# Kernel optimization log

Hardware: AMD Instinct MI355X
Metric: run time of the kernel (lower is better)

## Reference

```python
import jax, jax.numpy as jnp
import numpy as np

BN_EPS = 1e-5
NUM_HEADS = 8


def _bn(x, g, b, m, v):
    # eval-mode BatchNorm2d on NCHW
    inv = g / jnp.sqrt(v + BN_EPS)
    return x * inv[None, :, None, None] + (b - m * inv)[None, :, None, None]


def _l2norm_complex(t):
    # torch F.normalize(dim=-1) on complex: divide by L2 norm of magnitudes
    nrm = jnp.sqrt(jnp.sum(jnp.abs(t) ** 2, axis=-1, keepdims=True))
    return t / jnp.maximum(nrm, 1e-12)


def setup_inputs() -> dict:
    key = jax.random.key(0)
    ks = jax.random.split(key, 16)
    b, n, c = 8, 4096, 512
    dd = c // 2  # 256
    inp = {}
    inp['x'] = jax.random.normal(ks[0], (b, n, c), dtype=jnp.float32)
    inp['conv2_w'] = jax.random.normal(ks[1], (dd, c, 3, 3), dtype=jnp.float32) * 0.02
    inp['conv2_b'] = jax.random.normal(ks[2], (dd,), dtype=jnp.float32) * 0.02
    inp['bn2_g'] = jnp.ones((dd,), jnp.float32)
    inp['bn2_b'] = jnp.zeros((dd,), jnp.float32)
    inp['bn2_m'] = jax.random.normal(ks[3], (dd,), dtype=jnp.float32) * 0.1
    inp['bn2_v'] = jax.random.uniform(ks[4], (dd,), jnp.float32, 0.5, 1.5)
    inp['temperature'] = jnp.ones((NUM_HEADS, 1, 1), jnp.float32)
    hid = dd // 16  # 16
    inp['w1_w'] = jax.random.normal(ks[5], (hid, dd), dtype=jnp.float32) * 0.05
    inp['w1_b'] = jax.random.normal(ks[6], (hid,), dtype=jnp.float32) * 0.02
    inp['bnw_g'] = jnp.ones((hid,), jnp.float32)
    inp['bnw_b'] = jnp.zeros((hid,), jnp.float32)
    inp['bnw_m'] = jax.random.normal(ks[7], (hid,), dtype=jnp.float32) * 0.1
    inp['bnw_v'] = jax.random.uniform(ks[8], (hid,), jnp.float32, 0.5, 1.5)
    inp['w2_w'] = jax.random.normal(ks[9], (dd, hid), dtype=jnp.float32) * 0.05
    inp['w2_b'] = jax.random.normal(ks[10], (dd,), dtype=jnp.float32) * 0.02
    inp['proj_w'] = jax.random.normal(ks[11], (c, c), dtype=jnp.float32) * 0.02
    inp['proj_b'] = jax.random.normal(ks[12], (c,), dtype=jnp.float32) * 0.02
    return inp


def reference(x, conv2_w, conv2_b, bn2_g, bn2_b, bn2_m, bn2_v, temperature,
              w1_w, w1_b, bnw_g, bnw_b, bnw_m, bnw_v, w2_w, w2_b,
              proj_w, proj_b):
    b, n, c = x.shape
    h = w = int(round(n ** 0.5))
    x2d = x.reshape(b, h, w, c).transpose(0, 3, 1, 2)  # NCHW

    # conv2: 3x3 dilated (dilation=3, padding=3) -> BN -> ReLU
    conv2 = jax.lax.conv_general_dilated(
        x2d, conv2_w, window_strides=(1, 1), padding=((3, 3), (3, 3)),
        rhs_dilation=(3, 3), dimension_numbers=('NCHW', 'OIHW', 'NCHW'))
    conv2 = jax.nn.relu(_bn(conv2 + conv2_b[None, :, None, None], bn2_g, bn2_b, bn2_m, bn2_v))

    dd = conv2.shape[1]
    f = jnp.fft.fft2(conv2)  # q_f_2 = k_f_2 = v_f_2 = tepqkv (all identical)

    cph = dd // NUM_HEADS
    qkv = f.reshape(b, NUM_HEADS, cph, h * w)  # b head c (h w)
    qn = _l2norm_complex(qkv)  # q and k are identical after normalization

    # complex attention: (b,head,c,c)
    attn = jnp.einsum('bhcn,bhdn->bhcd', qn, qn) * temperature[None]
    attn = jax.lax.complex(jax.nn.softmax(attn.real, axis=-1),
                           jax.nn.softmax(attn.imag, axis=-1))
    out = jnp.einsum('bhcd,bhdn->bhcn', attn, qkv)
    # ifft2 over last two dims (c, h*w) as in the original code
    out_f2 = jnp.abs(jnp.fft.ifft2(out)).reshape(b, dd, h, w)

    # conv gating branch on real part of fft
    r = f.real
    g1 = jax.nn.relu(_bn(jnp.einsum('bchw,oc->bohw', r, w1_w) + w1_b[None, :, None, None],
                         bnw_g, bnw_b, bnw_m, bnw_v))
    gate = jax.nn.sigmoid(jnp.einsum('bchw,oc->bohw', g1, w2_w) + w2_b[None, :, None, None])
    out_l2 = jnp.abs(jnp.fft.ifft2(gate * f))

    out2 = jnp.concatenate([out_f2, out_l2], axis=1) + x2d
    F2 = jnp.einsum('bchw,oc->bohw', out2, proj_w) + proj_b[None, :, None, None]
    return F2.transpose(0, 2, 3, 1).reshape(b, n, c)
```

## Files before the change

### kernel.cpp

```cpp
#include <hip/hip_runtime.h>

#define NB 8
#define NC 512
#define ND 256
#define NP 4096
#define NHD 8
#define TWO_PI 6.2831853071795864f
#define FPITCH 65
#define HPAD 70
#define NSPL 16

typedef short bf16x8 __attribute__((ext_vector_type(8)));
typedef float f32x4 __attribute__((ext_vector_type(4)));

__device__ __forceinline__ unsigned short f2bf(float f) {
    unsigned u = __float_as_uint(f);
    u += 0x7FFFu + ((u >> 16) & 1u);
    return (unsigned short)(u >> 16);
}
__device__ __forceinline__ float bf2f(unsigned short u) {
    return __uint_as_float((unsigned)u << 16);
}

__device__ __forceinline__ void load_lds16(const void* g, void* l) {
// ... 64 lines not shown
    if (MODE == 0) {
        __syncthreads();
        #pragma unroll
        for (int k2 = 0; k2 < 8; ++k2) {
            int idx = r*FPITCH + t8 + 8*k2;
            Re[idx] = a[k2].x; Im[idx] = a[k2].y;
        }
    } else {
        #pragma unroll
        for (int k2 = 0; k2 < 8; ++k2) {
            int kq = t8 + 8*k2;
            gout[r + 64*kq] = make_float2(a[k2].x*scale, a[k2].y*scale);
        }
    }
    __syncthreads();
}

template<int S, int MODE>
__device__ void fft64_cols(float* Re, float* Im, const float* twc, const float* tws,
                           int tid, float* gre, float* gim, unsigned short* goutr,
                           float scale, float* ss)
{
    int col = tid & 63;
    int t8  = tid >> 6;
    float2 v[8];
    __syncthreads();
    #pragma unroll
    for (int m = 0; m < 8; ++m) {
        int idx = (8*m + t8)*FPITCH + col;
        v[m] = make_float2(Re[idx], Im[idx]);
    }
    dft8<S>(v);
    #pragma unroll
    for (int k1 = 1; k1 < 8; ++k1) {
        int mm = (t8*k1) & 63;
        v[k1] = cmulf(v[k1], make_float2(twc[mm], (float)S*tws[mm]));
    }
    __syncthreads();
    #pragma unroll
    for (int k1 = 0; k1 < 8; ++k1) {
        int idx = (k1*8 + t8)*FPITCH + col;
        Re[idx] = v[k1].x; Im[idx] = v[k1].y;
    }
    __syncthreads();
    float2 a[8];
    #pragma unroll
    for (int m = 0; m < 8; ++m) {
        int idx = (t8*8 + m)*FPITCH + col;
        a[m] = make_float2(Re[idx], Im[idx]);
    }
    dft8<S>(a);
    if (MODE <= 1) {
        __syncthreads();
        #pragma unroll
        for (int k2 = 0; k2 < 8; ++k2) {
            int row = t8 + 8*k2;
            float2 rv = a[k2];
            if (MODE == 1) {
                float sv, cv;
                __sincosf((TWO_PI/4096.f) * (float)(row*col), &sv, &cv);
                rv = cmulf(rv, make_float2(cv, (float)S*sv));
            }
            int idx = row*FPITCH + col;
            Re[idx] = rv.x; Im[idx] = rv.y;
        }
    } else if (MODE == 2) {
        #pragma unroll
        for (int k2 = 0; k2 < 8; ++k2) {
            int row = t8 + 8*k2;
            *ss += a[k2].x*a[k2].x + a[k2].y*a[k2].y;
            gre[row*64 + col] = a[k2].x*scale;
            gim[row*64 + col] = a[k2].y*scale;
        }
    } else {
        #pragma unroll
        for (int k2 = 0; k2 < 8; ++k2) {
            int row = t8 + 8*k2;
            goutr[row*64 + col] = f2bf(scale * sqrtf(a[k2].x*a[k2].x + a[k2].y*a[k2].y));
        }
    }
    __syncthreads();
}

__global__ __launch_bounds__(256) void k_wconv(const float* __restrict__ w, unsigned short* __restrict__ wB) {
    int idx = blockIdx.x*256 + threadIdx.x;
    if (idx >= 9*NC*ND) return;
    int i = idx & 511;
    int rest = idx >> 9;
    int o = rest & 255;
    int t = rest >> 8;
    wB[idx] = f2bf(w[(o*NC + i)*9 + t]);
}

__global__ __launch_bounds__(256) void k_wproj(const float* __restrict__ w, unsigned short* __restrict__ wb) {
    int i = blockIdx.x*256 + threadIdx.x;
    wb[i] = f2bf(w[i]);
}

__global__ __launch_bounds__(256) void k_xpad(const float* __restrict__ x, unsigned short* __restrict__ xpad) {
    int idx = blockIdx.x*256 + threadIdx.x;
    int c8 = idx & 63;
    int rest = idx >> 6;
    int wp = rest % HPAD;
    int rest2 = rest / HPAD;
    int hp = rest2 % HPAD;
    int b = rest2 / HPAD;
    int h = hp - 3, w = wp - 3;
    bf16x8 v = {0,0,0,0,0,0,0,0};
    if (((unsigned)h) < 64u && ((unsigned)w) < 64u) {
        const float* s = x + (((size_t)b*NP + h*64 + w)*NC + c8*8);
        float4 f0 = *(const float4*)(s);
        float4 f1 = *(const float4*)(s + 4);
        v[0]=(short)f2bf(f0.x); v[1]=(short)f2bf(f0.y); v[2]=(short)f2bf(f0.z); v[3]=(short)f2bf(f0.w);
        v[4]=(short)f2bf(f1.x); v[5]=(short)f2bf(f1.y); v[6]=(short)f2bf(f1.z); v[7]=(short)f2bf(f1.w);
    }
    *(bf16x8*)(xpad + ((size_t)(b*HPAD*HPAD) + hp*HPAD + wp)*NC + c8*8) = v;
}

__global__ __launch_bounds__(256, 2) void k_conv_mfma(
        const unsigned short* __restrict__ xpad, const unsigned short* __restrict__ wB,
        const float* __restrict__ cbias, const float* __restrict__ bg, const float* __restrict__ bb,
        const float* __restrict__ bm, const float* __restrict__ bv, float* __restrict__ out)
{
    __shared__ short Als[2][8192];
    __shared__ short Bls[2][8192];
    int tid = threadIdx.x;
    int p0 = blockIdx.x * 128;
    int o0 = blockIdx.y * 128;
    int b  = blockIdx.z;
    int lane = tid & 63;
    int wv = tid >> 6;
    int wr = wv >> 1, wc = wv & 1;
    int ln = lane & 15, kq = lane >> 4;
    int kqs = kq ^ ((ln >> 1) & 3);

    f32x4 acc[4][4];
    #pragma unroll
    for (int i = 0; i < 4; ++i)
        #pragma unroll
        for (int j = 0; j < 4; ++j)
            acc[i][j] = (f32x4){0.f, 0.f, 0.f, 0.f};

    int r0 = tid >> 2;
    int c16 = tid & 3;
    int c16s = c16 ^ ((r0 >> 1) & 3);
    int pA0 = p0 + r0, pA1 = p0 + 64 + r0;
    int h0 = pA0 >> 6, w0c = pA0 & 63;
    int h1 = pA1 >> 6, w1c = pA1 & 63;
    const unsigned short* xb = xpad + (size_t)b*(HPAD*HPAD)*NC;
    int oB0 = o0 + r0, oB1 = o0 + 64 + r0;
    short* AlsD0 = &Als[0][tid*8];
    short* AlsD1 = &Als[0][2048 + tid*8];
    short* BlsD0 = &Bls[0][tid*8];
    short* BlsD1 = &Bls[0][2048 + tid*8];

    auto stage = [&](int it) {
        int buf = it & 1;
        int tap = it >> 3;
        int kc  = (it & 7) << 6;
        int q   = (tap*11) >> 5;
        int dh  = q*3, dw = (tap - q*3)*3;
        const unsigned short* a0 = xb + ((size_t)((h0 + dh)*HPAD + (w0c + dw)))*NC + kc + c16s*8;
        const unsigned short* a1 = xb + ((size_t)((h1 + dh)*HPAD + (w1c + dw)))*NC + kc + c16s*8;
        const unsigned short* b0 = wB + ((size_t)(tap*ND + oB0))*NC + kc + c16s*8;
        const unsigned short* b1 = wB + ((size_t)(tap*ND + oB1))*NC + kc + c16s*8;
        int bo = buf ? 8192 : 0;
        load_lds16(a0,      AlsD0 + bo);
        load_lds16(a1,      AlsD1 + bo);
        load_lds16(a0 + 32, AlsD0 + bo + 4096);
        load_lds16(a1 + 32, AlsD1 + bo + 4096);
        load_lds16(b0,      BlsD0 + bo);
        load_lds16(b1,      BlsD1 + bo);
        load_lds16(b0 + 32, BlsD0 + bo + 4096);
        load_lds16(b1 + 32, BlsD1 + bo + 4096);
    };

    stage(0);
    #pragma unroll 2
    for (int it = 0; it < 72; ++it) {
        int buf = it & 1;
        asm volatile("s_waitcnt vmcnt(0)" ::: "memory");
        __builtin_amdgcn_s_barrier();
        __builtin_amdgcn_sched_barrier(0);
        if (it + 1 < 72) stage(it + 1);
        #pragma unroll
        for (int ks = 0; ks < 2; ++ks) {
            bf16x8 af[4], bfr[4];
            #pragma unroll
            for (int mi = 0; mi < 4; ++mi)
                af[mi] = *(const bf16x8*)&Als[buf][ks*4096 + (wr*64 + mi*16 + ln)*32 + kqs*8];
            #pragma unroll
            for (int ni = 0; ni < 4; ++ni)
                bfr[ni] = *(const bf16x8*)&Bls[buf][ks*4096 + (wc*64 + ni*16 + ln)*32 + kqs*8];
            #pragma unroll
            for (int mi = 0; mi < 4; ++mi)
                #pragma unroll
                for (int ni = 0; ni < 4; ++ni)
                    acc[mi][ni] = __builtin_amdgcn_mfma_f32_16x16x32_bf16(af[mi], bfr[ni], acc[mi][ni], 0, 0, 0);
        }
    }

    #pragma unroll
    for (int ni = 0; ni < 4; ++ni) {
        int o = o0 + wc*64 + ni*16 + ln;
        float inv = bg[o] * rsqrtf(bv[o] + 1e-5f);
        float beta = bb[o] - bm[o]*inv;
        float cbo = cbias[o];
        #pragma unroll
        for (int mi = 0; mi < 4; ++mi) {
            int p = p0 + wr*64 + mi*16 + kq*4;
            f32x4 v = acc[mi][ni];
            float4 rv;
            rv.x = fmaxf((v[0] + cbo)*inv + beta, 0.f);
            rv.y = fmaxf((v[1] + cbo)*inv + beta, 0.f);
            rv.z = fmaxf((v[2] + cbo)*inv + beta, 0.f);
            rv.w = fmaxf((v[3] + cbo)*inv + beta, 0.f);
            *(float4*)(out + ((size_t)(b*ND + o))*NP + p) = rv;
        }
    }
}

__global__ __launch_bounds__(512) void k_fft2_fwd(const float* __restrict__ src, float* __restrict__ fRe,
                                                  float* __restrict__ fIm, float* __restrict__ nrm) {
    __shared__ float Re[64*FPITCH];
    __shared__ float Im[64*FPITCH];
    __shared__ float twc[64], tws[64];
    __shared__ float part[8];
    int tid = threadIdx.x;
    size_t img = blockIdx.x;
    const float* s = src + img*4096;
    if (tid < 64) { float sv, cv; __sincosf(TWO_PI*(float)tid/64.f, &sv, &cv); twc[tid]=cv; tws[tid]=sv; }
    for (int i = tid; i < 4096; i += 512) {
        Re[(i>>6)*FPITCH + (i&63)] = s[i];
        Im[(i>>6)*FPITCH + (i&63)] = 0.f;
    }
    fft64_rows<-1,0>(Re, Im, twc, tws, tid, nullptr, 1.f);
    float ssl = 0.f;
    fft64_cols<-1,2>(Re, Im, twc, tws, tid, fRe + img*4096, fIm + img*4096, nullptr, 1.f, &ssl);
    #pragma unroll
    for (int off = 32; off > 0; off >>= 1) ssl += __shfl_down(ssl, off, 64);
    if ((tid & 63) == 0) part[tid >> 6] = ssl;
    __syncthreads();
    if (tid == 0) {
        float t = part[0]+part[1]+part[2]+part[3]+part[4]+part[5]+part[6]+part[7];
        nrm[img] = fmaxf(sqrtf(t), 1e-12f);
    }
}

__global__ __launch_bounds__(512) void k_ifft_row4096(const float* __restrict__ fRe,
        const float* __restrict__ fIm, float2* __restrict__ Z) {
    __shared__ float Re[64*FPITCH];
    __shared__ float Im[64*FPITCH];
    __shared__ float twc[64], tws[64];
    int tid = threadIdx.x;
    size_t img = blockIdx.x;
    const float* sr = fRe + img*4096;
    const float* si = fIm + img*4096;
    if (tid < 64) { float sv, cv; __sincosf(TWO_PI*(float)tid/64.f, &sv, &cv); twc[tid]=cv; tws[tid]=sv; }
    for (int i = tid; i < 4096; i += 512) {
        Re[(i>>6)*FPITCH + (i&63)] = sr[i];
        Im[(i>>6)*FPITCH + (i&63)] = si[i];
    }
    fft64_cols<1,1>(Re, Im, twc, tws, tid, nullptr, nullptr, nullptr, 1.f, nullptr);
    fft64_rows<1,1>(Re, Im, twc, tws, tid, Z + img*4096, 1.f/4096.f);
}

__global__ __launch_bounds__(512) void k_ifft2_abs_gated(const float* __restrict__ fRe,
        const float* __restrict__ fIm, const float* __restrict__ g1, const float* __restrict__ w2,
        const float* __restrict__ w2b, unsigned short* __restrict__ out) {
    __shared__ float Re[64*FPITCH];
    __shared__ float Im[64*FPITCH];
    __shared__ float twc[64], tws[64];
    int tid = threadIdx.x;
    size_t img = blockIdx.x;
    int b = (int)(img >> 8), ch = (int)(img & 255);
    const float* sr = fRe + img*4096;
    const float* si = fIm + img*4096;
    const float* g1b = g1 + (size_t)b*NP*16;
    float4 wv0 = *(const float4*)(w2 + ch*16);
    float4 wv1 = *(const float4*)(w2 + ch*16 + 4);
    float4 wv2 = *(const float4*)(w2 + ch*16 + 8);
    float4 wv3 = *(const float4*)(w2 + ch*16 + 12);
    float w2bias = w2b[ch];
    if (tid < 64) { float sv, cv; __sincosf(TWO_PI*(float)tid/64.f, &sv, &cv); twc[tid]=cv; tws[tid]=sv; }
    for (int i = tid; i < 4096; i += 512) {
        const float* gp = g1b + (size_t)i*16;
        float4 q0 = *(const float4*)(gp);
        float4 q1 = *(const float4*)(gp + 4);
        float4 q2 = *(const float4*)(gp + 8);
        float4 q3 = *(const float4*)(gp + 12);
        float acc = w2bias
            + wv0.x*q0.x + wv0.y*q0.y + wv0.z*q0.z + wv0.w*q0.w
            + wv1.x*q1.x + wv1.y*q1.y + wv1.z*q1.z + wv1.w*q1.w
            + wv2.x*q2.x + wv2.y*q2.y + wv2.z*q2.z + wv2.w*q2.w
            + wv3.x*q3.x + wv3.y*q3.y + wv3.z*q3.z + wv3.w*q3.w;
        float gate = 1.f / (1.f + __expf(-acc));
        Re[(i>>6)*FPITCH + (i&63)] = gate*sr[i];
        Im[(i>>6)*FPITCH + (i&63)] = gate*si[i];
    }
    fft64_rows<1,0>(Re, Im, twc, tws, tid, nullptr, 1.f);
    fft64_cols<1,3>(Re, Im, twc, tws, tid, nullptr, nullptr, out + img*4096, 1.f/4096.f, nullptr);
}

__global__ __launch_bounds__(256) void k_gram(const float* __restrict__ fRe, const float* __restrict__ fIm,
                                              float2* __restrict__ Gpart) {
    __shared__ short FrP[32*136];
    __shared__ short FiP[32*136];
    int split = blockIdx.x;
    int bh = blockIdx.y;
    int b = bh >> 3, h = bh & 7;
    int tid = threadIdx.x;
    int lane = tid & 63;
    int wv = tid >> 6;
    int cr = (wv >> 1) * 16, dc = (wv & 1) * 16;
    int ln = lane & 15, kq = lane >> 4;
    int r = tid >> 3;
    int g = tid & 7;
    const float* fRb = fRe + ((size_t)(b*ND + h*32) + r)*NP + split*256 + g*8;
    const float* fIb = fIm + ((size_t)(b*ND + h*32) + r)*NP + split*256 + g*8;
    short* wFr = FrP + r*136 + g*16;
    short* wFi = FiP + r*136 + g*16;

    f32x4 arr = {0.f,0.f,0.f,0.f}, aii = {0.f,0.f,0.f,0.f};
    f32x4 ari = {0.f,0.f,0.f,0.f}, air = {0.f,0.f,0.f,0.f};

    for (int chunk = 0; chunk < 4; ++chunk) {
        float4 v0 = *(const float4*)(fRb + chunk*64);
        float4 v1 = *(const float4*)(fRb + chunk*64 + 4);
        float4 w0 = *(const float4*)(fIb + chunk*64);
        float4 w1 = *(const float4*)(fIb + chunk*64 + 4);
        __syncthreads();
        float vr[8] = {v0.x,v0.y,v0.z,v0.w,v1.x,v1.y,v1.z,v1.w};
        float vi[8] = {w0.x,w0.y,w0.z,w0.w,w1.x,w1.y,w1.z,w1.w};
        bf16x8 r0v, r1v, i0v, i1v;
        #pragma unroll
        for (int j = 0; j < 4; ++j) {
            unsigned short hb;
            hb = f2bf(vr[j]);   r0v[2*j] = (short)hb; r0v[2*j+1] = (short)f2bf(vr[j]   - bf2f(hb));
            hb = f2bf(vr[4+j]); r1v[2*j] = (short)hb; r1v[2*j+1] = (short)f2bf(vr[4+j] - bf2f(hb));
            hb = f2bf(vi[j]);   i0v[2*j] = (short)hb; i0v[2*j+1] = (short)f2bf(vi[j]   - bf2f(hb));
            hb = f2bf(vi[4+j]); i1v[2*j] = (short)hb; i1v[2*j+1] = (short)f2bf(vi[4+j] - bf2f(hb));
        }
        *(bf16x8*)(wFr)     = r0v;
        *(bf16x8*)(wFr + 8) = r1v;
        *(bf16x8*)(wFi)     = i0v;
        *(bf16x8*)(wFi + 8) = i1v;
        __syncthreads();
        const short* aRp = FrP + (cr + ln)*136;
        const short* aIp = FiP + (cr + ln)*136;
        const short* bRp = FrP + (dc + ln)*136;
        const short* bIp = FiP + (dc + ln)*136;
        #pragma unroll
        for (int s = 0; s < 4; ++s) {
            int ko = s*32 + kq*8;
            bf16x8 aR = *(const bf16x8*)(aRp + ko);
            bf16x8 aI = *(const bf16x8*)(aIp + ko);
            bf16x8 bR = *(const bf16x8*)(bRp + ko);
            bf16x8 bI = *(const bf16x8*)(bIp + ko);
            arr = __builtin_amdgcn_mfma_f32_16x16x32_bf16(aR, bR, arr, 0, 0, 0);
            aii = __builtin_amdgcn_mfma_f32_16x16x32_bf16(aI, bI, aii, 0, 0, 0);
            ari = __builtin_amdgcn_mfma_f32_16x16x32_bf16(aR, bI, ari, 0, 0, 0);
            air = __builtin_amdgcn_mfma_f32_16x16x32_bf16(aI, bR, air, 0, 0, 0);
        }
    }
    float2* gout = Gpart + ((size_t)bh*NSPL + split)*1024;
    #pragma unroll
    for (int j = 0; j < 4; ++j) {
        int c = cr + kq*4 + j;
        int d = dc + ln;
        gout[c*32 + d] = make_float2(arr[j] - aii[j], ari[j] + air[j]);
    }
}

__global__ __launch_bounds__(256) void k_attn(const float2* __restrict__ Gpart, const float* __restrict__ nrm,
                                              const float* __restrict__ temp, float2* __restrict__ Ap) {
    int bh = blockIdx.x;
    int b = bh >> 3, h = bh & 7;
    int tid = threadIdx.x;
    __shared__ float2 Sm[32][33];
    __shared__ float twc[32], tws[32];
    if (tid < 32) { float sv, cv; __sincosf(TWO_PI*(float)tid/32.f, &sv, &cv); twc[tid]=cv; tws[tid]=sv; }
    const float* nb = nrm + b*ND + h*32;
    float tv = temp[h];
    const float2* gp = Gpart + (size_t)bh*NSPL*1024;
    #pragma unroll
    for (int j = 0; j < 4; ++j) {
        int e = tid*4 + j;
        int c = e >> 5, d = e & 31;
        float2 s = make_float2(0.f, 0.f);
        for (int sp = 0; sp < NSPL; ++sp) { float2 v = gp[sp*1024 + e]; s.x += v.x; s.y += v.y; }
        float sc = tv / (nb[c]*nb[d]);
        Sm[c][d] = make_float2(s.x*sc, s.y*sc);
    }
    __syncthreads();
    if (tid < 32) {
        float mr = -1e30f, mi = -1e30f;
        for (int d = 0; d < 32; ++d) { float2 v = Sm[tid][d]; mr = fmaxf(mr, v.x); mi = fmaxf(mi, v.y); }
        float sr = 0.f, si = 0.f;
        for (int d = 0; d < 32; ++d) {
            float2 v = Sm[tid][d];
            v.x = __expf(v.x - mr); v.y = __expf(v.y - mi);
            sr += v.x; si += v.y;
            Sm[tid][d] = v;
        }
        float ir = 1.f/sr, ii = 1.f/si;
        for (int d = 0; d < 32; ++d) { float2 v = Sm[tid][d]; Sm[tid][d] = make_float2(v.x*ir, v.y*ii); }
    }
    __syncthreads();
    float2* ap = Ap + (size_t)bh*1024;
    #pragma unroll
    for (int j = 0; j < 4; ++j) {
        int e = tid*4 + j;
        int k = e >> 5, d = e & 31;
        float2 acc = make_float2(0.f, 0.f);
        for (int c = 0; c < 32; ++c) {
            int m = (c*k) & 31;
            float2 w = make_float2(twc[m], tws[m]);
            float2 v = Sm[c][d];
            acc.x += w.x*v.x - w.y*v.y;
            acc.y += w.x*v.y + w.y*v.x;
        }
        ap[e] = make_float2(acc.x*(1.f/32.f), acc.y*(1.f/32.f));
    }
}

__global__ __launch_bounds__(256) void k_outf2(const float2* __restrict__ Ap, const float2* __restrict__ Z,
                                               unsigned short* __restrict__ outf2) {
    __shared__ short Are[32*136], Aim[32*136];
    __shared__ short Bre[64*136], Bim[64*136];
    int nchunk = blockIdx.x, bh = blockIdx.y;
    int b = bh >> 3, h = bh & 7;
    int n0 = nchunk * 64;
    int tid = threadIdx.x;
    int lane = tid & 63;
    int wv = tid >> 6;
    int ln = lane & 15, kq = lane >> 4;

    const float2* ap = Ap + (size_t)bh*1024;
    #pragma unroll
    for (int j = 0; j < 4; ++j) {
        int e = tid*4 + j;
        int c = e >> 5, d = e & 31;
        float2 a = ap[e];
        unsigned short rh = f2bf(a.x); unsigned short rl = f2bf(a.x - bf2f(rh));
        unsigned short ih = f2bf(a.y); unsigned short il = f2bf(a.y - bf2f(ih));
        short* pr = Are + c*136 + 4*d;
        short* pi = Aim + c*136 + 4*d;
        pr[0]=(short)rh; pr[1]=(short)rh; pr[2]=(short)rl; pr[3]=(short)rl;
        pi[0]=(short)ih; pi[1]=(short)ih; pi[2]=(short)il; pi[3]=(short)il;
    }
    const float2* zb = Z + ((size_t)(b*ND + h*32))*NP + n0;
    #pragma unroll
    for (int j = 0; j < 8; ++j) {
        int e = tid + 256*j;
        int d = e >> 6, n = e & 63;
        float2 z = zb[(size_t)d*NP + n];
        unsigned short rh = f2bf(z.x); unsigned short rl = f2bf(z.x - bf2f(rh));
        unsigned short ih = f2bf(z.y); unsigned short il = f2bf(z.y - bf2f(ih));
        short* pr = Bre + n*136 + 4*d;
        short* pi = Bim + n*136 + 4*d;
        pr[0]=(short)rh; pr[1]=(short)rl; pr[2]=(short)rh; pr[3]=(short)rl;
        pi[0]=(short)ih; pi[1]=(short)il; pi[2]=(short)ih; pi[3]=(short)il;
    }
    __syncthreads();

    f32x4 arr[2], aii[2], ari[2], air[2];
    #pragma unroll
    for (int mt = 0; mt < 2; ++mt) {
        arr[mt] = (f32x4){0.f,0.f,0.f,0.f}; aii[mt] = (f32x4){0.f,0.f,0.f,0.f};
        ari[mt] = (f32x4){0.f,0.f,0.f,0.f}; air[mt] = (f32x4){0.f,0.f,0.f,0.f};
    }
    const short* bRrow = Bre + (wv*16 + ln)*136;
    const short* bIrow = Bim + (wv*16 + ln)*136;
    #pragma unroll
    for (int s = 0; s < 4; ++s) {
        int ko = s*32 + kq*8;
        bf16x8 bR = *(const bf16x8*)(bRrow + ko);
        bf16x8 bI = *(const bf16x8*)(bIrow + ko);
        #pragma unroll
        for (int mt = 0; mt < 2; ++mt) {
            bf16x8 aR = *(const bf16x8*)(Are + (mt*16 + ln)*136 + ko);
            bf16x8 aI = *(const bf16x8*)(Aim + (mt*16 + ln)*136 + ko);
            arr[mt] = __builtin_amdgcn_mfma_f32_16x16x32_bf16(aR, bR, arr[mt], 0, 0, 0);
            aii[mt] = __builtin_amdgcn_mfma_f32_16x16x32_bf16(aI, bI, aii[mt], 0, 0, 0);
            ari[mt] = __builtin_amdgcn_mfma_f32_16x16x32_bf16(aR, bI, ari[mt], 0, 0, 0);
            air[mt] = __builtin_amdgcn_mfma_f32_16x16x32_bf16(aI, bR, air[mt], 0, 0, 0);
        }
    }
    #pragma unroll
    for (int mt = 0; mt < 2; ++mt)
        #pragma unroll
        for (int j = 0; j < 4; ++j) {
            int c = mt*16 + kq*4 + j;
            float re = arr[mt][j] - aii[mt][j];
            float im = ari[mt][j] + air[mt][j];
            outf2[((size_t)(b*ND + h*32 + c))*NP + n0 + wv*16 + ln] = f2bf(sqrtf(re*re + im*im));
        }
}

__global__ __launch_bounds__(256) void k_g1(const float* __restrict__ fRe, const float* __restrict__ w1,
        const float* __restrict__ w1b, const float* __restrict__ gg, const float* __restrict__ gb,
        const float* __restrict__ gm, const float* __restrict__ gv, float* __restrict__ g1)
{
    int pc = blockIdx.x, b = blockIdx.y;
    int tid = threadIdx.x;
    __shared__ float w1s[16*256];
    for (int i = tid; i < 4096; i += 256) w1s[i] = w1[i];
    __syncthreads();
    int p = pc*256 + tid;
    const float* fb = fRe + (size_t)b*ND*NP + p;
    float acc[16];
    #pragma unroll
    for (int j = 0; j < 16; ++j) acc[j] = 0.f;
    for (int i = 0; i < 256; ++i) {
        float v = fb[(size_t)i*NP];
        #pragma unroll
        for (int j = 0; j < 16; ++j) acc[j] += w1s[j*256 + i] * v;
    }
    float* go = g1 + ((size_t)b*NP + p)*16;
    float4 o4[4];
    #pragma unroll
    for (int j = 0; j < 16; ++j) {
        float inv = gg[j]*rsqrtf(gv[j] + 1e-5f);
        float val = (acc[j] + w1b[j])*inv + (gb[j] - gm[j]*inv);
        ((float*)o4)[j] = fmaxf(val, 0.f);
    }
    *(float4*)(go)      = o4[0];
    *(float4*)(go + 4)  = o4[1];
    *(float4*)(go + 8)  = o4[2];
    *(float4*)(go + 12) = o4[3];
}

__global__ __launch_bounds__(256) void k_prep(const unsigned short* __restrict__ outf2b,
        const unsigned short* __restrict__ outl2b, const float* __restrict__ x,
        unsigned short* __restrict__ A)
{
    int tid = threadIdx.x;
    int p = blockIdx.x*64 + (tid >> 2);
    int cs = blockIdx.y*64 + (tid & 3)*16;
    int b  = blockIdx.z;
    const unsigned short* src = (cs < ND) ? (outf2b + ((size_t)(b*ND) + cs)*NP + p)
                                          : (outl2b + ((size_t)(b*ND) + (cs - ND))*NP + p);
    float av[16];
    #pragma unroll
    for (int j = 0; j < 16; ++j) av[j] = bf2f(src[(size_t)j*NP]);
    const float* xp = x + ((size_t)(b*NP) + p)*NC + cs;
    #pragma unroll
    for (int j = 0; j < 4; ++j) {
        float4 xv = *(const float4*)(xp + j*4);
        av[j*4+0] += xv.x; av[j*4+1] += xv.y; av[j*4+2] += xv.z; av[j*4+3] += xv.w;
    }
    bf16x8 v0, v1;
    #pragma unroll
    for (int j = 0; j < 8; ++j) { v0[j] = (short)f2bf(av[j]); v1[j] = (short)f2bf(av[8+j]); }
    unsigned short* ap = A + ((size_t)(b*NP) + p)*NC + cs;
    *(bf16x8*)(ap) = v0;
    *(bf16x8*)(ap + 8) = v1;
}

__global__ __launch_bounds__(256, 2) void k_projm(
        const unsigned short* __restrict__ A, const unsigned short* __restrict__ Bw,
        const float* __restrict__ pb, float* __restrict__ out)
{
    __shared__ short Als[2][8192];
    __shared__ short Bls[2][8192];
    int tid = threadIdx.x;
    int p0 = blockIdx.x * 128;
    int o0 = blockIdx.y * 128;
    int b  = blockIdx.z;
    int lane = tid & 63;
    int wv = tid >> 6;
    int wr = wv >> 1, wc = wv & 1;
    int ln = lane & 15, kq = lane >> 4;
    int kqs = kq ^ ((ln >> 1) & 3);

    f32x4 acc[4][4];
    #pragma unroll
    for (int i = 0; i < 4; ++i)
        #pragma unroll
        for (int j = 0; j < 4; ++j)
            acc[i][j] = (f32x4){0.f, 0.f, 0.f, 0.f};

    int r0 = tid >> 2;
    int c16 = tid & 3;
    int c16s = c16 ^ ((r0 >> 1) & 3);
    const unsigned short* ga0 = A + ((size_t)(b*NP) + p0 + r0)*NC + c16s*8;
    const unsigned short* ga1 = A + ((size_t)(b*NP) + p0 + 64 + r0)*NC + c16s*8;
    const unsigned short* gb0 = Bw + (size_t)(o0 + r0)*NC + c16s*8;
    const unsigned short* gb1 = Bw + (size_t)(o0 + 64 + r0)*NC + c16s*8;
    short* AlsD0 = &Als[0][tid*8];
    short* AlsD1 = &Als[0][2048 + tid*8];
    short* BlsD0 = &Bls[0][tid*8];
    short* BlsD1 = &Bls[0][2048 + tid*8];

    auto stage = [&](int it) {
        int buf = it & 1;
        int kc = it << 6;
        int bo = buf ? 8192 : 0;
        load_lds16(ga0 + kc,      AlsD0 + bo);
        load_lds16(ga1 + kc,      AlsD1 + bo);
        load_lds16(ga0 + kc + 32, AlsD0 + bo + 4096);
        load_lds16(ga1 + kc + 32, AlsD1 + bo + 4096);
        load_lds16(gb0 + kc,      BlsD0 + bo);
        load_lds16(gb1 + kc,      BlsD1 + bo);
        load_lds16(gb0 + kc + 32, BlsD0 + bo + 4096);
        load_lds16(gb1 + kc + 32, BlsD1 + bo + 4096);
    };

    stage(0);
    #pragma unroll 2
    for (int it = 0; it < 8; ++it) {
        int buf = it & 1;
        asm volatile("s_waitcnt vmcnt(0)" ::: "memory");
        __builtin_amdgcn_s_barrier();
        __builtin_amdgcn_sched_barrier(0);
        if (it + 1 < 8) stage(it + 1);
        #pragma unroll
        for (int ks = 0; ks < 2; ++ks) {
            bf16x8 af[4], bfr[4];
            #pragma unroll
            for (int mi = 0; mi < 4; ++mi)
                af[mi] = *(const bf16x8*)&Als[buf][ks*4096 + (wr*64 + mi*16 + ln)*32 + kqs*8];
            #pragma unroll
            for (int ni = 0; ni < 4; ++ni)
                bfr[ni] = *(const bf16x8*)&Bls[buf][ks*4096 + (wc*64 + ni*16 + ln)*32 + kqs*8];
            #pragma unroll
            for (int mi = 0; mi < 4; ++mi)
                #pragma unroll
                for (int ni = 0; ni < 4; ++ni)
                    acc[mi][ni] = __builtin_amdgcn_mfma_f32_16x16x32_bf16(af[mi], bfr[ni], acc[mi][ni], 0, 0, 0);
        }
    }

    #pragma unroll
    for (int ni = 0; ni < 4; ++ni) {
        int o = o0 + wc*64 + ni*16 + ln;
        float bias = pb[o];
        #pragma unroll
        for (int mi = 0; mi < 4; ++mi) {
            int p = p0 + wr*64 + mi*16 + kq*4;
            f32x4 v = acc[mi][ni];
            float* op = out + ((size_t)(b*NP) + p)*NC + o;
            op[0]        = v[0] + bias;
            op[NC]       = v[1] + bias;
            op[2*NC]     = v[2] + bias;
            op[3*(size_t)NC] = v[3] + bias;
        }
    }
}

extern "C" void kernel_launch(void* const* d_in, const int* in_sizes, int n_in,
                              void* d_out, int out_size, void* d_ws, size_t ws_size,
                              hipStream_t stream)
{
    const float* x      = (const float*)d_in[0];
    const float* conv_w = (const float*)d_in[1];
    const float* conv_b = (const float*)d_in[2];
    const float* bn2g   = (const float*)d_in[3];
    const float* bn2b   = (const float*)d_in[4];
    const float* bn2m   = (const float*)d_in[5];
    const float* bn2v   = (const float*)d_in[6];
    const float* temp   = (const float*)d_in[7];
    const float* w1w    = (const float*)d_in[8];
    const float* w1b    = (const float*)d_in[9];
    const float* bnwg   = (const float*)d_in[10];
    const float* bnwb   = (const float*)d_in[11];
    const float* bnwm   = (const float*)d_in[12];
    const float* bnwv   = (const float*)d_in[13];
    const float* w2w    = (const float*)d_in[14];
    const float* w2b    = (const float*)d_in[15];
    const float* projw  = (const float*)d_in[16];
    const float* projb  = (const float*)d_in[17];
    float* out = (float*)d_out;

    char* ws = (char*)d_ws;
    unsigned short* wB = (unsigned short*)(ws);
    float*  nrm   = (float*)(ws);
    float2* Ap    = (float2*)(ws + 8192 + 4194304);
    float*  g1    = (float*)(ws + 8192 + 4194304 + 524288);
    char* base = ws + 6823936;
    float*  conv  = (float*)(base);
    unsigned short* outf2b = (unsigned short*)(base);
    float* fRe = (float*)(base + 33554432);
    float* fIm = (float*)(base + 33554432 + 33554432);
    unsigned short* xpad = (unsigned short*)(base + 33554432);
    char* zbase = base + 33554432 + 67108864;
    float2* Gpart = (float2*)(zbase);
    float2* Z     = (float2*)(zbase);
    unsigned short* pwb = (unsigned short*)(zbase);
    unsigned short* Abf = (unsigned short*)(zbase + 4194304);
    unsigned short* outl2b = (unsigned short*)(zbase + 37748736);

    k_wconv<<<dim3(4608), 256, 0, stream>>>(conv_w, wB);
    k_xpad<<<dim3(9800), 256, 0, stream>>>(x, xpad);
    k_conv_mfma<<<dim3(32, 2, 8), 256, 0, stream>>>(xpad, wB, conv_b, bn2g, bn2b, bn2m, bn2v, conv);
    k_fft2_fwd<<<dim3(2048), 512, 0, stream>>>(conv, fRe, fIm, nrm);
    k_gram<<<dim3(NSPL, 64), 256, 0, stream>>>(fRe, fIm, Gpart);
    k_attn<<<dim3(64), 256, 0, stream>>>(Gpart, nrm, temp, Ap);
    k_ifft_row4096<<<dim3(2048), 512, 0, stream>>>(fRe, fIm, Z);
    k_outf2<<<dim3(64, 64), 256, 0, stream>>>(Ap, Z, outf2b);
    k_g1<<<dim3(16, 8), 256, 0, stream>>>(fRe, w1w, w1b, bnwg, bnwb, bnwm, bnwv, g1);
    k_ifft2_abs_gated<<<dim3(2048), 512, 0, stream>>>(fRe, fIm, g1, w2w, w2b, outl2b);
    k_wproj<<<dim3(1024), 256, 0, stream>>>(projw, pwb);
    k_prep<<<dim3(64, 8, 8), 256, 0, stream>>>(outf2b, outl2b, x, Abf);
    k_projm<<<dim3(32, 4, 8), 256, 0, stream>>>(Abf, pwb, projb, out);
}
```

Baseline: 425.5 us.

## Merge independent small kernels into block-range dispatched launches

Result: slower. 446.9 us (+5.0%).

```diff
diff --git a/kernel.cpp b/kernel.cpp
--- a/kernel.cpp
+++ b/kernel.cpp
@@ -170,39 +170,42 @@
     __syncthreads();
 }
 
-__global__ __launch_bounds__(256) void k_wconv(const float* __restrict__ w, unsigned short* __restrict__ wB) {
-    int idx = blockIdx.x*256 + threadIdx.x;
-    if (idx >= 9*NC*ND) return;
-    int i = idx & 511;
-    int rest = idx >> 9;
-    int o = rest & 255;
-    int t = rest >> 8;
-    wB[idx] = f2bf(w[(o*NC + i)*9 + t]);
-}
-
-__global__ __launch_bounds__(256) void k_wproj(const float* __restrict__ w, unsigned short* __restrict__ wb) {
-    int i = blockIdx.x*256 + threadIdx.x;
-    wb[i] = f2bf(w[i]);
-}
-
-__global__ __launch_bounds__(256) void k_xpad(const float* __restrict__ x, unsigned short* __restrict__ xpad) {
-    int idx = blockIdx.x*256 + threadIdx.x;
-    int c8 = idx & 63;
-    int rest = idx >> 6;
-    int wp = rest % HPAD;
-    int rest2 = rest / HPAD;
-    int hp = rest2 % HPAD;
-    int b = rest2 / HPAD;
-    int h = hp - 3, w = wp - 3;
-    bf16x8 v = {0,0,0,0,0,0,0,0};
-    if (((unsigned)h) < 64u && ((unsigned)w) < 64u) {
-        const float* s = x + (((size_t)b*NP + h*64 + w)*NC + c8*8);
-        float4 f0 = *(const float4*)(s);
-        float4 f1 = *(const float4*)(s + 4);
-        v[0]=(short)f2bf(f0.x); v[1]=(short)f2bf(f0.y); v[2]=(short)f2bf(f0.z); v[3]=(short)f2bf(f0.w);
-        v[4]=(short)f2bf(f1.x); v[5]=(short)f2bf(f1.y); v[6]=(short)f2bf(f1.z); v[7]=(short)f2bf(f1.w);
-    }
-    *(bf16x8*)(xpad + ((size_t)(b*HPAD*HPAD) + hp*HPAD + wp)*NC + c8*8) = v;
+__global__ __launch_bounds__(256) void k_pre(const float* __restrict__ cw, const float* __restrict__ pw,
+        const float* __restrict__ x, unsigned short* __restrict__ wB,
+        unsigned short* __restrict__ pwb, unsigned short* __restrict__ xpad)
+{
+    int bid = blockIdx.x;
+    int tid = threadIdx.x;
+    if (bid < 4608) {
+        int idx = bid*256 + tid;
+        if (idx >= 9*NC*ND) return;
+        int i = idx & 511;
+        int rest = idx >> 9;
+        int o = rest & 255;
+        int t = rest >> 8;
+        wB[idx] = f2bf(cw[(o*NC + i)*9 + t]);
+    } else if (bid < 5632) {
+        int i = (bid - 4608)*256 + tid;
+        pwb[i] = f2bf(pw[i]);
+    } else {
+        int idx = (bid - 5632)*256 + tid;
+        int c8 = idx & 63;
+        int rest = idx >> 6;
+        int wp = rest % HPAD;
+        int rest2 = rest / HPAD;
+        int hp = rest2 % HPAD;
+        int b = rest2 / HPAD;
+        int h = hp - 3, w = wp - 3;
+        bf16x8 v = {0,0,0,0,0,0,0,0};
+        if (((unsigned)h) < 64u && ((unsigned)w) < 64u) {
+            const float* s = x + (((size_t)b*NP + h*64 + w)*NC + c8*8);
+            float4 f0 = *(const float4*)(s);
+            float4 f1 = *(const float4*)(s + 4);
+            v[0]=(short)f2bf(f0.x); v[1]=(short)f2bf(f0.y); v[2]=(short)f2bf(f0.z); v[3]=(short)f2bf(f0.w);
+            v[4]=(short)f2bf(f1.x); v[5]=(short)f2bf(f1.y); v[6]=(short)f2bf(f1.z); v[7]=(short)f2bf(f1.w);
+        }
+        *(bf16x8*)(xpad + ((size_t)(b*HPAD*HPAD) + hp*HPAD + wp)*NC + c8*8) = v;
+    }
 }
 
 __global__ __launch_bounds__(256, 2) void k_conv_mfma(
@@ -335,180 +338,211 @@
     }
 }
 
-__global__ __launch_bounds__(512) void k_ifft_row4096(const float* __restrict__ fRe,
-        const float* __restrict__ fIm, float2* __restrict__ Z) {
-    __shared__ float Re[64*FPITCH];
-    __shared__ float Im[64*FPITCH];
-    __shared__ float twc[64], tws[64];
+__global__ __launch_bounds__(256) void k_gram_g1(const float* __restrict__ fRe, const float* __restrict__ fIm,
+        float2* __restrict__ Gpart, const float* __restrict__ w1, const float* __restrict__ w1b,
+        const float* __restrict__ gg, const float* __restrict__ gb, const float* __restrict__ gm,
+        const float* __restrict__ gv, float* __restrict__ g1)
+{
+    __shared__ __align__(16) float smemF[4352];
+    int bid = blockIdx.x;
     int tid = threadIdx.x;
-    size_t img = blockIdx.x;
-    const float* sr = fRe + img*4096;
-    const float* si = fIm + img*4096;
-    if (tid < 64) { float sv, cv; __sincosf(TWO_PI*(float)tid/64.f, &sv, &cv); twc[tid]=cv; tws[tid]=sv; }
-    for (int i = tid; i < 4096; i += 512) {
-        Re[(i>>6)*FPITCH + (i&63)] = sr[i];
-        Im[(i>>6)*FPITCH + (i&63)] = si[i];
-    }
-    fft64_cols<1,1>(Re, Im, twc, tws, tid, nullptr, nullptr, nullptr, 1.f, nullptr);
-    fft64_rows<1,1>(Re, Im, twc, tws, tid, Z + img*4096, 1.f/4096.f);
-}
-
-__global__ __launch_bounds__(512) void k_ifft2_abs_gated(const float* __restrict__ fRe,
-        const float* __restrict__ fIm, const float* __restrict__ g1, const float* __restrict__ w2,
-        const float* __restrict__ w2b, unsigned short* __restrict__ out) {
-    __shared__ float Re[64*FPITCH];
-    __shared__ float Im[64*FPITCH];
-    __shared__ float twc[64], tws[64];
+    if (bid < 1024) {
+        short* FrP = (short*)smemF;
+        short* FiP = ((short*)smemF) + 32*136;
+        int split = bid & 15;
+        int bh = bid >> 4;
+        int b = bh >> 3, h = bh & 7;
+        int lane = tid & 63;
+        int wv = tid >> 6;
+        int cr = (wv >> 1) * 16, dc = (wv & 1) * 16;
+        int ln = lane & 15, kq = lane >> 4;
+        int r = tid >> 3;
+        int g = tid & 7;
+        const float* fRb = fRe + ((size_t)(b*ND + h*32) + r)*NP + split*256 + g*8;
+        const float* fIb = fIm + ((size_t)(b*ND + h*32) + r)*NP + split*256 + g*8;
+        short* wFr = FrP + r*136 + g*16;
+        short* wFi = FiP + r*136 + g*16;
+
+        f32x4 arr = {0.f,0.f,0.f,0.f}, aii = {0.f,0.f,0.f,0.f};
+        f32x4 ari = {0.f,0.f,0.f,0.f}, air = {0.f,0.f,0.f,0.f};
+
+        for (int chunk = 0; chunk < 4; ++chunk) {
+            float4 v0 = *(const float4*)(fRb + chunk*64);
+            float4 v1 = *(const float4*)(fRb + chunk*64 + 4);
+            float4 w0 = *(const float4*)(fIb + chunk*64);
+            float4 w1v = *(const float4*)(fIb + chunk*64 + 4);
+            __syncthreads();
+            float vr[8] = {v0.x,v0.y,v0.z,v0.w,v1.x,v1.y,v1.z,v1.w};
+            float vi[8] = {w0.x,w0.y,w0.z,w0.w,w1v.x,w1v.y,w1v.z,w1v.w};
+            bf16x8 r0v, r1v, i0v, i1v;
+            #pragma unroll
+            for (int j = 0; j < 4; ++j) {
+                unsigned short hb;
+                hb = f2bf(vr[j]);   r0v[2*j] = (short)hb; r0v[2*j+1] = (short)f2bf(vr[j]   - bf2f(hb));
+                hb = f2bf(vr[4+j]); r1v[2*j] = (short)hb; r1v[2*j+1] = (short)f2bf(vr[4+j] - bf2f(hb));
+                hb = f2bf(vi[j]);   i0v[2*j] = (short)hb; i0v[2*j+1] = (short)f2bf(vi[j]   - bf2f(hb));
+                hb = f2bf(vi[4+j]); i1v[2*j] = (short)hb; i1v[2*j+1] = (short)f2bf(vi[4+j] - bf2f(hb));
+            }
+            *(bf16x8*)(wFr)     = r0v;
+            *(bf16x8*)(wFr + 8) = r1v;
+            *(bf16x8*)(wFi)     = i0v;
+            *(bf16x8*)(wFi + 8) = i1v;
+            __syncthreads();
+            const short* aRp = FrP + (cr + ln)*136;
+            const short* aIp = FiP + (cr + ln)*136;
+            const short* bRp = FrP + (dc + ln)*136;
+            const short* bIp = FiP + (dc + ln)*136;
+            #pragma unroll
+            for (int s = 0; s < 4; ++s) {
+                int ko = s*32 + kq*8;
+                bf16x8 aR = *(const bf16x8*)(aRp + ko);
+                bf16x8 aI = *(const bf16x8*)(aIp + ko);
+                bf16x8 bR = *(const bf16x8*)(bRp + ko);
+                bf16x8 bI = *(const bf16x8*)(bIp + ko);
+                arr = __builtin_amdgcn_mfma_f32_16x16x32_bf16(aR, bR, arr, 0, 0, 0);
+                aii = __builtin_amdgcn_mfma_f32_16x16x32_bf16(aI, bI, aii, 0, 0, 0);
+                ari = __builtin_amdgcn_mfma_f32_16x16x32_bf16(aR, bI, ari, 0, 0, 0);
+                air = __builtin_amdgcn_mfma_f32_16x16x32_bf16(aI, bR, air, 0, 0, 0);
+            }
+        }
+        float2* gout = Gpart + ((size_t)bh*NSPL + split)*1024;
+        #pragma unroll
+        for (int j = 0; j < 4; ++j) {
+            int c = cr + kq*4 + j;
+            int d = dc + ln;
+            gout[c*32 + d] = make_float2(arr[j] - aii[j], ari[j] + air[j]);
+        }
+    } else {
+        float* w1s = smemF;
+        int rr = bid - 1024;
+        int pc = rr & 15, b = rr >> 4;
+        for (int i = tid; i < 4096; i += 256) w1s[i] = w1[i];
+        __syncthreads();
+        int p = pc*256 + tid;
+        const float* fb = fRe + (size_t)b*ND*NP + p;
+        float acc[16];
+        #pragma unroll
+        for (int j = 0; j < 16; ++j) acc[j] = 0.f;
+        for (int i = 0; i < 256; ++i) {
+            float v = fb[(size_t)i*NP];
+            #pragma unroll
+            for (int j = 0; j < 16; ++j) acc[j] += w1s[j*256 + i] * v;
+        }
+        float* go = g1 + ((size_t)b*NP + p)*16;
+        float4 o4[4];
+        #pragma unroll
+        for (int j = 0; j < 16; ++j) {
+            float inv = gg[j]*rsqrtf(gv[j] + 1e-5f);
+            float val = (acc[j] + w1b[j])*inv + (gb[j] - gm[j]*inv);
+            ((float*)o4)[j] = fmaxf(val, 0.f);
+        }
+        *(float4*)(go)      = o4[0];
+        *(float4*)(go + 4)  = o4[1];
+        *(float4*)(go + 8)  = o4[2];
+        *(float4*)(go + 12) = o4[3];
+    }
+}
+
+__global__ __launch_bounds__(512) void k_mid(const float2* __restrict__ Gpart, const float* __restrict__ nrm,
+        const float* __restrict__ temp, float2* __restrict__ Ap,
+        const float* __restrict__ fRe, const float* __restrict__ fIm, float2* __restrict__ Z,
+        const float* __restrict__ g1, const float* __restrict__ w2, const float* __restrict__ w2b,
+        unsigned short* __restrict__ outl2b)
+{
+    __shared__ __align__(16) float S[8448];
+    float* Re  = S;
+    float* Im  = S + 4160;
+    float* twc = S + 8320;
+    float* tws = S + 8384;
+    int bid = blockIdx.x;
     int tid = threadIdx.x;
-    size_t img = blockIdx.x;
-    int b = (int)(img >> 8), ch = (int)(img & 255);
-    const float* sr = fRe + img*4096;
-    const float* si = fIm + img*4096;
-    const float* g1b = g1 + (size_t)b*NP*16;
-    float4 wv0 = *(const float4*)(w2 + ch*16);
-    float4 wv1 = *(const float4*)(w2 + ch*16 + 4);
-    float4 wv2 = *(const float4*)(w2 + ch*16 + 8);
-    float4 wv3 = *(const float4*)(w2 + ch*16 + 12);
-    float w2bias = w2b[ch];
-    if (tid < 64) { float sv, cv; __sincosf(TWO_PI*(float)tid/64.f, &sv, &cv); twc[tid]=cv; tws[tid]=sv; }
-    for (int i = tid; i < 4096; i += 512) {
-        const float* gp = g1b + (size_t)i*16;
-        float4 q0 = *(const float4*)(gp);
-        float4 q1 = *(const float4*)(gp + 4);
-        float4 q2 = *(const float4*)(gp + 8);
-        float4 q3 = *(const float4*)(gp + 12);
-        float acc = w2bias
-            + wv0.x*q0.x + wv0.y*q0.y + wv0.z*q0.z + wv0.w*q0.w
-            + wv1.x*q1.x + wv1.y*q1.y + wv1.z*q1.z + wv1.w*q1.w
-            + wv2.x*q2.x + wv2.y*q2.y + wv2.z*q2.z + wv2.w*q2.w
-            + wv3.x*q3.x + wv3.y*q3.y + wv3.z*q3.z + wv3.w*q3.w;
-        float gate = 1.f / (1.f + __expf(-acc));
-        Re[(i>>6)*FPITCH + (i&63)] = gate*sr[i];
-        Im[(i>>6)*FPITCH + (i&63)] = gate*si[i];
-    }
-    fft64_rows<1,0>(Re, Im, twc, tws, tid, nullptr, 1.f);
-    fft64_cols<1,3>(Re, Im, twc, tws, tid, nullptr, nullptr, out + img*4096, 1.f/4096.f, nullptr);
-}
-
-__global__ __launch_bounds__(256) void k_gram(const float* __restrict__ fRe, const float* __restrict__ fIm,
-                                              float2* __restrict__ Gpart) {
-    __shared__ short FrP[32*136];
-    __shared__ short FiP[32*136];
-    int split = blockIdx.x;
-    int bh = blockIdx.y;
-    int b = bh >> 3, h = bh & 7;
-    int tid = threadIdx.x;
-    int lane = tid & 63;
-    int wv = tid >> 6;
-    int cr = (wv >> 1) * 16, dc = (wv & 1) * 16;
-    int ln = lane & 15, kq = lane >> 4;
-    int r = tid >> 3;
-    int g = tid & 7;
-    const float* fRb = fRe + ((size_t)(b*ND + h*32) + r)*NP + split*256 + g*8;
-    const float* fIb = fIm + ((size_t)(b*ND + h*32) + r)*NP + split*256 + g*8;
-    short* wFr = FrP + r*136 + g*16;
-    short* wFi = FiP + r*136 + g*16;
-
-    f32x4 arr = {0.f,0.f,0.f,0.f}, aii = {0.f,0.f,0.f,0.f};
-    f32x4 ari = {0.f,0.f,0.f,0.f}, air = {0.f,0.f,0.f,0.f};
-
-    for (int chunk = 0; chunk < 4; ++chunk) {
-        float4 v0 = *(const float4*)(fRb + chunk*64);
-        float4 v1 = *(const float4*)(fRb + chunk*64 + 4);
-        float4 w0 = *(const float4*)(fIb + chunk*64);
-        float4 w1 = *(const float4*)(fIb + chunk*64 + 4);
+    if (bid < 64) {
+        float2* Sm = (float2*)S;
+        int bh = bid;
+        int b = bh >> 3, h = bh & 7;
+        if (tid < 32) { float sv, cv; __sincosf(TWO_PI*(float)tid/32.f, &sv, &cv); twc[tid]=cv; tws[tid]=sv; }
+        const float* nb = nrm + b*ND + h*32;
+        float tv = temp[h];
+        const float2* gp = Gpart + (size_t)bh*NSPL*1024;
+        #pragma unroll
+        for (int j = 0; j < 2; ++j) {
+            int e = tid*2 + j;
+            int c = e >> 5, d = e & 31;
+            float2 s = make_float2(0.f, 0.f);
+            for (int sp = 0; sp < NSPL; ++sp) { float2 v = gp[sp*1024 + e]; s.x += v.x; s.y += v.y; }
+            float sc = tv / (nb[c]*nb[d]);
+            Sm[c*33 + d] = make_float2(s.x*sc, s.y*sc);
+        }
         __syncthreads();
-        float vr[8] = {v0.x,v0.y,v0.z,v0.w,v1.x,v1.y,v1.z,v1.w};
-        float vi[8] = {w0.x,w0.y,w0.z,w0.w,w1.x,w1.y,w1.z,w1.w};
-        bf16x8 r0v, r1v, i0v, i1v;
-        #pragma unroll
-        for (int j = 0; j < 4; ++j) {
-            unsigned short hb;
-            hb = f2bf(vr[j]);   r0v[2*j] = (short)hb; r0v[2*j+1] = (short)f2bf(vr[j]   - bf2f(hb));
-            hb = f2bf(vr[4+j]); r1v[2*j] = (short)hb; r1v[2*j+1] = (short)f2bf(vr[4+j] - bf2f(hb));
-            hb = f2bf(vi[j]);   i0v[2*j] = (short)hb; i0v[2*j+1] = (short)f2bf(vi[j]   - bf2f(hb));
-            hb = f2bf(vi[4+j]); i1v[2*j] = (short)hb; i1v[2*j+1] = (short)f2bf(vi[4+j] - bf2f(hb));
-        }
-        *(bf16x8*)(wFr)     = r0v;
-        *(bf16x8*)(wFr + 8) = r1v;
-        *(bf16x8*)(wFi)     = i0v;
-        *(bf16x8*)(wFi + 8) = i1v;
+        if (tid < 32) {
+            float mr = -1e30f, mi = -1e30f;
+            for (int d = 0; d < 32; ++d) { float2 v = Sm[tid*33 + d]; mr = fmaxf(mr, v.x); mi = fmaxf(mi, v.y); }
+            float sr = 0.f, si = 0.f;
+            for (int d = 0; d < 32; ++d) {
+                float2 v = Sm[tid*33 + d];
+                v.x = __expf(v.x - mr); v.y = __expf(v.y - mi);
+                sr += v.x; si += v.y;
+                Sm[tid*33 + d] = v;
+            }
+            float ir = 1.f/sr, ii = 1.f/si;
+            for (int d = 0; d < 32; ++d) { float2 v = Sm[tid*33 + d]; Sm[tid*33 + d] = make_float2(v.x*ir, v.y*ii); }
+        }
         __syncthreads();
-        const short* aRp = FrP + (cr + ln)*136;
-        const short* aIp = FiP + (cr + ln)*136;
-        const short* bRp = FrP + (dc + ln)*136;
-        const short* bIp = FiP + (dc + ln)*136;
-        #pragma unroll
-        for (int s = 0; s < 4; ++s) {
-            int ko = s*32 + kq*8;
-            bf16x8 aR = *(const bf16x8*)(aRp + ko);
-            bf16x8 aI = *(const bf16x8*)(aIp + ko);
-            bf16x8 bR = *(const bf16x8*)(bRp + ko);
-            bf16x8 bI = *(const bf16x8*)(bIp + ko);
-            arr = __builtin_amdgcn_mfma_f32_16x16x32_bf16(aR, bR, arr, 0, 0, 0);
-            aii = __builtin_amdgcn_mfma_f32_16x16x32_bf16(aI, bI, aii, 0, 0, 0);
-            ari = __builtin_amdgcn_mfma_f32_16x16x32_bf16(aR, bI, ari, 0, 0, 0);
-            air = __builtin_amdgcn_mfma_f32_16x16x32_bf16(aI, bR, air, 0, 0, 0);
-        }
-    }
-    float2* gout = Gpart + ((size_t)bh*NSPL + split)*1024;
-    #pragma unroll
-    for (int j = 0; j < 4; ++j) {
-        int c = cr + kq*4 + j;
-        int d = dc + ln;
-        gout[c*32 + d] = make_float2(arr[j] - aii[j], ari[j] + air[j]);
-    }
-}
-
-__global__ __launch_bounds__(256) void k_attn(const float2* __restrict__ Gpart, const float* __restrict__ nrm,
-                                              const float* __restrict__ temp, float2* __restrict__ Ap) {
-    int bh = blockIdx.x;
-    int b = bh >> 3, h = bh & 7;
-    int tid = threadIdx.x;
-    __shared__ float2 Sm[32][33];
-    __shared__ float twc[32], tws[32];
-    if (tid < 32) { float sv, cv; __sincosf(TWO_PI*(float)tid/32.f, &sv, &cv); twc[tid]=cv; tws[tid]=sv; }
-    const float* nb = nrm + b*ND + h*32;
-    float tv = temp[h];
-    const float2* gp = Gpart + (size_t)bh*NSPL*1024;
-    #pragma unroll
-    for (int j = 0; j < 4; ++j) {
-        int e = tid*4 + j;
-        int c = e >> 5, d = e & 31;
-        float2 s = make_float2(0.f, 0.f);
-        for (int sp = 0; sp < NSPL; ++sp) { float2 v = gp[sp*1024 + e]; s.x += v.x; s.y += v.y; }
-        float sc = tv / (nb[c]*nb[d]);
-        Sm[c][d] = make_float2(s.x*sc, s.y*sc);
-    }
-    __syncthreads();
-    if (tid < 32) {
-        float mr = -1e30f, mi = -1e30f;
-        for (int d = 0; d < 32; ++d) { float2 v = Sm[tid][d]; mr = fmaxf(mr, v.x); mi = fmaxf(mi, v.y); }
-        float sr = 0.f, si = 0.f;
-        for (int d = 0; d < 32; ++d) {
-            float2 v = Sm[tid][d];
-            v.x = __expf(v.x - mr); v.y = __expf(v.y - mi);
-            sr += v.x; si += v.y;
-            Sm[tid][d] = v;
-        }
-        float ir = 1.f/sr, ii = 1.f/si;
-        for (int d = 0; d < 32; ++d) { float2 v = Sm[tid][d]; Sm[tid][d] = make_float2(v.x*ir, v.y*ii); }
-    }
-    __syncthreads();
-    float2* ap = Ap + (size_t)bh*1024;
-    #pragma unroll
-    for (int j = 0; j < 4; ++j) {
-        int e = tid*4 + j;
-        int k = e >> 5, d = e & 31;
-        float2 acc = make_float2(0.f, 0.f);
-        for (int c = 0; c < 32; ++c) {
-            int m = (c*k) & 31;
-            float2 w = make_float2(twc[m], tws[m]);
-            float2 v = Sm[c][d];
-            acc.x += w.x*v.x - w.y*v.y;
-            acc.y += w.x*v.y + w.y*v.x;
-        }
-        ap[e] = make_float2(acc.x*(1.f/32.f), acc.y*(1.f/32.f));
+        float2* ap = Ap + (size_t)bh*1024;
+        #pragma unroll
+        for (int j = 0; j < 2; ++j) {
+            int e = tid*2 + j;
+            int k = e >> 5, d = e & 31;
+            float2 acc = make_float2(0.f, 0.f);
+            for (int c = 0; c < 32; ++c) {
+                int m = (c*k) & 31;
+                float2 w = make_float2(twc[m], tws[m]);
+                float2 v = Sm[c*33 + d];
+                acc.x += w.x*v.x - w.y*v.y;
+                acc.y += w.x*v.y + w.y*v.x;
+            }
+            ap[e] = make_float2(acc.x*(1.f/32.f), acc.y*(1.f/32.f));
+        }
+    } else if (bid < 2112) {
+        size_t img = bid - 64;
+        const float* sr = fRe + img*4096;
+        const float* si = fIm + img*4096;
+        if (tid < 64) { float sv, cv; __sincosf(TWO_PI*(float)tid/64.f, &sv, &cv); twc[tid]=cv; tws[tid]=sv; }
+        for (int i = tid; i < 4096; i += 512) {
+            Re[(i>>6)*FPITCH + (i&63)] = sr[i];
+            Im[(i>>6)*FPITCH + (i&63)] = si[i];
+        }
+        fft64_cols<1,1>(Re, Im, twc, tws, tid, nullptr, nullptr, nullptr, 1.f, nullptr);
+        fft64_rows<1,1>(Re, Im, twc, tws, tid, Z + img*4096, 1.f/4096.f);
+    } else {
+        size_t img = bid - 2112;
+        int b = (int)(img >> 8), ch = (int)(img & 255);
+        const float* sr = fRe + img*4096;
+        const float* si = fIm + img*4096;
+        const float* g1b = g1 + (size_t)b*NP*16;
+        float4 wv0 = *(const float4*)(w2 + ch*16);
+        float4 wv1 = *(const float4*)(w2 + ch*16 + 4);
+        float4 wv2 = *(const float4*)(w2 + ch*16 + 8);
+        float4 wv3 = *(const float4*)(w2 + ch*16 + 12);
+        float w2bias = w2b[ch];
+        if (tid < 64) { float sv, cv; __sincosf(TWO_PI*(float)tid/64.f, &sv, &cv); twc[tid]=cv; tws[tid]=sv; }
+        for (int i = tid; i < 4096; i += 512) {
+            const float* gp = g1b + (size_t)i*16;
+            float4 q0 = *(const float4*)(gp);
+            float4 q1 = *(const float4*)(gp + 4);
+            float4 q2 = *(const float4*)(gp + 8);
+            float4 q3 = *(const float4*)(gp + 12);
+            float acc = w2bias
+                + wv0.x*q0.x + wv0.y*q0.y + wv0.z*q0.z + wv0.w*q0.w
+                + wv1.x*q1.x + wv1.y*q1.y + wv1.z*q1.z + wv1.w*q1.w
+                + wv2.x*q2.x + wv2.y*q2.y + wv2.z*q2.z + wv2.w*q2.w
+                + wv3.x*q3.x + wv3.y*q3.y + wv3.z*q3.z + wv3.w*q3.w;
+            float gate = 1.f / (1.f + __expf(-acc));
+            Re[(i>>6)*FPITCH + (i&63)] = gate*sr[i];
+            Im[(i>>6)*FPITCH + (i&63)] = gate*si[i];
+        }
+        fft64_rows<1,0>(Re, Im, twc, tws, tid, nullptr, 1.f);
+        fft64_cols<1,3>(Re, Im, twc, tws, tid, nullptr, nullptr, outl2b + img*4096, 1.f/4096.f, nullptr);
     }
 }
 
@@ -586,39 +620,6 @@
         }
 }
 
-__global__ __launch_bounds__(256) void k_g1(const float* __restrict__ fRe, const float* __restrict__ w1,
-        const float* __restrict__ w1b, const float* __restrict__ gg, const float* __restrict__ gb,
-        const float* __restrict__ gm, const float* __restrict__ gv, float* __restrict__ g1)
-{
-    int pc = blockIdx.x, b = blockIdx.y;
-    int tid = threadIdx.x;
-    __shared__ float w1s[16*256];
-    for (int i = tid; i < 4096; i += 256) w1s[i] = w1[i];
-    __syncthreads();
-    int p = pc*256 + tid;
-    const float* fb = fRe + (size_t)b*ND*NP + p;
-    float acc[16];
-    #pragma unroll
-    for (int j = 0; j < 16; ++j) acc[j] = 0.f;
-    for (int i = 0; i < 256; ++i) {
-        float v = fb[(size_t)i*NP];
-        #pragma unroll
-        for (int j = 0; j < 16; ++j) acc[j] += w1s[j*256 + i] * v;
-    }
-    float* go = g1 + ((size_t)b*NP + p)*16;
-    float4 o4[4];
-    #pragma unroll
-    for (int j = 0; j < 16; ++j) {
-        float inv = gg[j]*rsqrtf(gv[j] + 1e-5f);
-        float val = (acc[j] + w1b[j])*inv + (gb[j] - gm[j]*inv);
-        ((float*)o4)[j] = fmaxf(val, 0.f);
-    }
-    *(float4*)(go)      = o4[0];
-    *(float4*)(go + 4)  = o4[1];
-    *(float4*)(go + 8)  = o4[2];
-    *(float4*)(go + 12) = o4[3];
-}
-
 __global__ __launch_bounds__(256) void k_prep(const unsigned short* __restrict__ outf2b,
         const unsigned short* __restrict__ outl2b, const float* __restrict__ x,
         unsigned short* __restrict__ A)
@@ -644,6 +645,11 @@
     unsigned short* ap = A + ((size_t)(b*NP) + p)*NC + cs;
     *(bf16x8*)(ap) = v0;
     *(bf16x8*)(ap + 8) = v1;
+}
+
+__global__ __launch_bounds__(256) void k_wproj(const float* __restrict__ w, unsigned short* __restrict__ wb) {
+    int i = blockIdx.x*256 + threadIdx.x;
+    wb[i] = f2bf(w[i]);
 }
 
 __global__ __launch_bounds__(256, 2) void k_projm(
@@ -768,27 +774,23 @@
     float*  g1    = (float*)(ws + 8192 + 4194304 + 524288);
     char* base = ws + 6823936;
     float*  conv  = (float*)(base);
-    unsigned short* outf2b = (unsigned short*)(base);
+    unsigned short* outl2b = (unsigned short*)(base);
+    float2* Gpart = (float2*)(base + 16777216);
+    unsigned short* outf2b = (unsigned short*)(base + 16777216);
     float* fRe = (float*)(base + 33554432);
     float* fIm = (float*)(base + 33554432 + 33554432);
     unsigned short* xpad = (unsigned short*)(base + 33554432);
     char* zbase = base + 33554432 + 67108864;
-    float2* Gpart = (float2*)(zbase);
     float2* Z     = (float2*)(zbase);
     unsigned short* pwb = (unsigned short*)(zbase);
     unsigned short* Abf = (unsigned short*)(zbase + 4194304);
-    unsigned short* outl2b = (unsigned short*)(zbase + 37748736);
-
-    k_wconv<<<dim3(4608), 256, 0, stream>>>(conv_w, wB);
-    k_xpad<<<dim3(9800), 256, 0, stream>>>(x, xpad);
+
+    k_pre<<<dim3(15432), 256, 0, stream>>>(conv_w, projw, x, wB, pwb, xpad);
     k_conv_mfma<<<dim3(32, 2, 8), 256, 0, stream>>>(xpad, wB, conv_b, bn2g, bn2b, bn2m, bn2v, conv);
     k_fft2_fwd<<<dim3(2048), 512, 0, stream>>>(conv, fRe, fIm, nrm);
-    k_gram<<<dim3(NSPL, 64), 256, 0, stream>>>(fRe, fIm, Gpart);
-    k_attn<<<dim3(64), 256, 0, stream>>>(Gpart, nrm, temp, Ap);
-    k_ifft_row4096<<<dim3(2048), 512, 0, stream>>>(fRe, fIm, Z);
+    k_gram_g1<<<dim3(1152), 256, 0, stream>>>(fRe, fIm, Gpart, w1w, w1b, bnwg, bnwb, bnwm, bnwv, g1);
+    k_mid<<<dim3(4160), 512, 0, stream>>>(Gpart, nrm, temp, Ap, fRe, fIm, Z, g1, w2w, w2b, outl2b);
     k_outf2<<<dim3(64, 64), 256, 0, stream>>>(Ap, Z, outf2b);
-    k_g1<<<dim3(16, 8), 256, 0, stream>>>(fRe, w1w, w1b, bnwg, bnwb, bnwm, bnwv, g1);
-    k_ifft2_abs_gated<<<dim3(2048), 512, 0, stream>>>(fRe, fIm, g1, w2w, w2b, outl2b);
     k_wproj<<<dim3(1024), 256, 0, stream>>>(projw, pwb);
     k_prep<<<dim3(64, 8, 8), 256, 0, stream>>>(outf2b, outl2b, x, Abf);
     k_projm<<<dim3(32, 4, 8), 256, 0, stream>>>(Abf, pwb, projb, out);
```
